# Kernel tuning notes

Measured on AMD Instinct MI355X. Metric: run time of the kernel, lower is better.

The kernel has to match this reference:

```python
import jax, jax.numpy as jnp
import numpy as np

# Dense grid configuration (B, D, H, W) and channels C = nPlanes
B, D, H, W = 4, 64, 64, 64
C = 32
N_ACTIVE = 400000
N_SITES = B * D * H * W  # 1048576


def setup_inputs() -> dict:
    key = jax.random.key(0)
    k1, k2 = jax.random.split(key)
    features = jax.random.normal(k1, (N_ACTIVE, C), dtype=jnp.float32)
    flat_idx = jax.random.randint(k2, (N_ACTIVE,), 0, N_SITES, dtype=jnp.int64)
    return {"features": features, "flat_idx": flat_idx}


def reference(features, flat_idx):
    # Scatter sparse voxel features into the dense grid.
    # features: [N_active, C]; flat_idx: [N_active] linear index into B*D*H*W sites.
    dense = jnp.zeros((N_SITES, C), dtype=features.dtype)
    dense = dense.at[flat_idx].add(features)  # active sites are unique -> add == set
    # [B*D*H*W, C] -> [B, C, D, H, W] to match SCN's NCDHW dense layout
    return dense.reshape(B, D, H, W, C).transpose(0, 4, 1, 2, 3)
```

## Files before the change

kernel.cpp:

```cpp
#include <hip/hip_runtime.h>


#define DHW_LOG2 18
#define DHW (1 << DHW_LOG2)
#define C_CH 32
#define N_SITES_TOTAL (4 * DHW)
#define SITES_PER_BLOCK 128
#define LDS_PAD 132

typedef float floatx4 __attribute__((ext_vector_type(4)));

__global__ __launch_bounds__(256) void init_head_kernel(int* __restrict__ head, int n)
{
    int t = blockIdx.x * blockDim.x + threadIdx.x;
    if (t < n) head[t] = -1;
}

__global__ __launch_bounds__(256) void build_chains_kernel(
    const int* __restrict__ flat_idx,
    int* __restrict__ head,
    int* __restrict__ next,
    int n_active)
{
    int i = blockIdx.x * blockDim.x + threadIdx.x;
    if (i >= n_active) return;
    int s = flat_idx[i];
    int prev = atomicExch(&head[s], i);
    next[i] = prev;
}

__global__ __launch_bounds__(256) void gather_kernel(
    const float* __restrict__ feats,
    const int* __restrict__ head,
    const int* __restrict__ next,
    float* __restrict__ out)
{
    __shared__ __align__(16) float lds[C_CH][LDS_PAD];

    const int t  = threadIdx.x;
    const int sl = t >> 1;
    const int h  = t & 1;
    const int S0 = blockIdx.x * SITES_PER_BLOCK;
    const int S  = S0 + sl;

    floatx4 a0 = (floatx4)0.f, a1 = (floatx4)0.f, a2 = (floatx4)0.f, a3 = (floatx4)0.f;

    int p = head[S];
    while (p != -1) {
        const floatx4* row = (const floatx4*)(feats + ((size_t)p * C_CH + h * 16));
        int pn = next[p];
        floatx4 f0 = row[0];
        floatx4 f1 = row[1];
        floatx4 f2 = row[2];
        floatx4 f3 = row[3];
        a0 += f0; a1 += f1; a2 += f2; a3 += f3;
        p = pn;
    }

    float acc[16] = {
        a0.x, a0.y, a0.z, a0.w,  a1.x, a1.y, a1.z, a1.w,
        a2.x, a2.y, a2.z, a2.w,  a3.x, a3.y, a3.z, a3.w };
    #pragma unroll
    for (int j = 0; j < 16; ++j)
        lds[h * 16 + j][sl] = acc[j];

    __syncthreads();

    const int b   = S0 >> DHW_LOG2;
    const int sp0 = S0 & (DHW - 1);
    #pragma unroll
    for (int it = 0; it < 4; ++it) {
        int q  = it * 256 + t;
        int c  = q >> 5;
        int i4 = q & 31;
        floatx4 v = *reinterpret_cast<const floatx4*>(&lds[c][i4 * 4]);
        floatx4* o = reinterpret_cast<floatx4*>(
            out + (((size_t)(b * C_CH + c)) << DHW_LOG2) + sp0 + i4 * 4);
        __builtin_nontemporal_store(v, o);
    }
}

__global__ __launch_bounds__(256) void zero_kernel(float4* __restrict__ out, int n4)
{
    int t = blockIdx.x * blockDim.x + threadIdx.x;
    if (t < n4) out[t] = make_float4(0.f, 0.f, 0.f, 0.f);
}

__global__ __launch_bounds__(256) void scatter_atomic_kernel(
    const float* __restrict__ feats,
    const int* __restrict__ flat_idx,
    float* __restrict__ out,
    int n_active)
{
    int t = blockIdx.x * blockDim.x + threadIdx.x;
    int i = t >> 5, c = t & 31;
    if (i >= n_active) return;
    int s = flat_idx[i];
    atomicAdd(&out[(((size_t)(s >> DHW_LOG2) * C_CH + c) << DHW_LOG2) + (s & (DHW - 1))],
              feats[(size_t)i * C_CH + c]);
}

extern "C" void kernel_launch(void* const* d_in, const int* in_sizes, int n_in,
                              void* d_out, int out_size, void* d_ws, size_t ws_size,
                              hipStream_t stream) {
    const float* feats = (const float*)d_in[0];
    const int*   idx   = (const int*)d_in[1];
    float*       out   = (float*)d_out;
    int n_active = in_sizes[1];

    size_t head_bytes = (size_t)N_SITES_TOTAL * sizeof(int);
    size_t next_bytes = (size_t)n_active * sizeof(int);

    if (ws_size >= head_bytes + next_bytes) {
        int* head = (int*)d_ws;
        int* next = (int*)((char*)d_ws + head_bytes);

        init_head_kernel<<<(N_SITES_TOTAL + 255) / 256, 256, 0, stream>>>(head, N_SITES_TOTAL);
        build_chains_kernel<<<(n_active + 255) / 256, 256, 0, stream>>>(idx, head, next, n_active);
        gather_kernel<<<N_SITES_TOTAL / SITES_PER_BLOCK, 256, 0, stream>>>(feats, head, next, out);
    } else {
        int n4 = out_size >> 2;
        zero_kernel<<<(n4 + 255) / 256, 256, 0, stream>>>((float4*)out, n4);
        int total = n_active * C_CH;
        scatter_atomic_kernel<<<(total + 255) / 256, 256, 0, stream>>>(feats, idx, out, n_active);
    }
}
```

Measured before the change: 201.8 us.

## Replace per-site linked lists with fixed-capacity buckets plus overflow chain

Replaces the atomicExch linked-list chains with per-site count arrays and 8-slot buckets, with a linked-list fallback for overflow. The gather kernel loads up to eight row indices with two vector loads and issues the feature loads independently. This removes the serial dependent next[] pointer chase. The cost is a larger workspace (32 MB of buckets), extra init work for the count array, and a bucket read for every site, including empty ones.

```diff
diff --git a/kernel.cpp b/kernel.cpp
--- a/kernel.cpp
+++ b/kernel.cpp
@@ -6,33 +6,48 @@
 #define C_CH 32
 #define N_SITES_TOTAL (4 * DHW)
 #define SITES_PER_BLOCK 128
+#define N_TILES (N_SITES_TOTAL / SITES_PER_BLOCK)
 #define LDS_PAD 132
+#define CAP 8
 
 typedef float floatx4 __attribute__((ext_vector_type(4)));
 
-__global__ __launch_bounds__(256) void init_head_kernel(int* __restrict__ head, int n)
+__global__ __launch_bounds__(256) void init_kernel(int* __restrict__ count,
+                                                   int* __restrict__ ovf_head)
 {
     int t = blockIdx.x * blockDim.x + threadIdx.x;
-    if (t < n) head[t] = -1;
+    if (t < N_SITES_TOTAL / 2) {
+        ((int2*)count)[t]    = make_int2(0, 0);
+        ((int2*)ovf_head)[t] = make_int2(-1, -1);
+    }
 }
 
-__global__ __launch_bounds__(256) void build_chains_kernel(
+__global__ __launch_bounds__(256) void fill_buckets_kernel(
     const int* __restrict__ flat_idx,
-    int* __restrict__ head,
-    int* __restrict__ next,
+    int* __restrict__ count,
+    int* __restrict__ bucket,
+    int* __restrict__ ovf_head,
+    int* __restrict__ ovf_next,
     int n_active)
 {
     int i = blockIdx.x * blockDim.x + threadIdx.x;
     if (i >= n_active) return;
     int s = flat_idx[i];
-    int prev = atomicExch(&head[s], i);
-    next[i] = prev;
+    int pos = atomicAdd(&count[s], 1);
+    if (pos < CAP) {
+        bucket[(size_t)s * CAP + pos] = i;
+    } else {
+        int prev = atomicExch(&ovf_head[s], i);
+        ovf_next[i] = prev;
+    }
 }
 
 __global__ __launch_bounds__(256) void gather_kernel(
     const float* __restrict__ feats,
-    const int* __restrict__ head,
-    const int* __restrict__ next,
+    const int* __restrict__ count,
+    const int* __restrict__ bucket,
+    const int* __restrict__ ovf_head,
+    const int* __restrict__ ovf_next,
     float* __restrict__ out)
 {
     __shared__ __align__(16) float lds[C_CH][LDS_PAD];
@@ -43,18 +58,38 @@
     const int S0 = blockIdx.x * SITES_PER_BLOCK;
     const int S  = S0 + sl;
 
+    int c = count[S];
+    const int4* bkt = (const int4*)(bucket + (size_t)S * CAP);
+    int4 b0 = bkt[0];
+    int4 b1 = bkt[1];
+
     floatx4 a0 = (floatx4)0.f, a1 = (floatx4)0.f, a2 = (floatx4)0.f, a3 = (floatx4)0.f;
 
-    int p = head[S];
-    while (p != -1) {
-        const floatx4* row = (const floatx4*)(feats + ((size_t)p * C_CH + h * 16));
-        int pn = next[p];
-        floatx4 f0 = row[0];
-        floatx4 f1 = row[1];
-        floatx4 f2 = row[2];
-        floatx4 f3 = row[3];
-        a0 += f0; a1 += f1; a2 += f2; a3 += f3;
-        p = pn;
+    const int rows[CAP] = { b0.x, b0.y, b0.z, b0.w, b1.x, b1.y, b1.z, b1.w };
+    #pragma unroll
+    for (int k = 0; k < CAP; ++k) {
+        if (k < c) {
+            const floatx4* row = (const floatx4*)(feats + ((size_t)rows[k] * C_CH + h * 16));
+            floatx4 f0 = row[0];
+            floatx4 f1 = row[1];
+            floatx4 f2 = row[2];
+            floatx4 f3 = row[3];
+            a0 += f0; a1 += f1; a2 += f2; a3 += f3;
+        }
+    }
+
+    if (c > CAP) {
+        int p = ovf_head[S];
+        while (p != -1) {
+            const floatx4* row = (const floatx4*)(feats + ((size_t)p * C_CH + h * 16));
+            int pn = ovf_next[p];
+            floatx4 f0 = row[0];
+            floatx4 f1 = row[1];
+            floatx4 f2 = row[2];
+            floatx4 f3 = row[3];
+            a0 += f0; a1 += f1; a2 += f2; a3 += f3;
+            p = pn;
+        }
     }
 
     float acc[16] = {
@@ -71,11 +106,11 @@
     #pragma unroll
     for (int it = 0; it < 4; ++it) {
         int q  = it * 256 + t;
-        int c  = q >> 5;
+        int cc = q >> 5;
         int i4 = q & 31;
-        floatx4 v = *reinterpret_cast<const floatx4*>(&lds[c][i4 * 4]);
+        floatx4 v = *reinterpret_cast<const floatx4*>(&lds[cc][i4 * 4]);
         floatx4* o = reinterpret_cast<floatx4*>(
-            out + (((size_t)(b * C_CH + c)) << DHW_LOG2) + sp0 + i4 * 4);
+            out + (((size_t)(b * C_CH + cc)) << DHW_LOG2) + sp0 + i4 * 4);
         __builtin_nontemporal_store(v, o);
     }
 }
@@ -108,16 +143,23 @@
     float*       out   = (float*)d_out;
     int n_active = in_sizes[1];
 
-    size_t head_bytes = (size_t)N_SITES_TOTAL * sizeof(int);
-    size_t next_bytes = (size_t)n_active * sizeof(int);
+    size_t count_bytes = (size_t)N_SITES_TOTAL * sizeof(int);
+    size_t head_bytes  = (size_t)N_SITES_TOTAL * sizeof(int);
+    size_t next_bytes  = ((size_t)n_active * sizeof(int) + 0xFFFFF) & ~(size_t)0xFFFFF;
+    size_t bucket_off  = count_bytes + head_bytes + next_bytes;
+    size_t bucket_bytes = (size_t)N_SITES_TOTAL * CAP * sizeof(int);
 
-    if (ws_size >= head_bytes + next_bytes) {
-        int* head = (int*)d_ws;
-        int* next = (int*)((char*)d_ws + head_bytes);
+    if (ws_size >= bucket_off + bucket_bytes) {
+        int* count    = (int*)d_ws;
+        int* ovf_head = (int*)((char*)d_ws + count_bytes);
+        int* ovf_next = (int*)((char*)d_ws + count_bytes + head_bytes);
+        int* bucket   = (int*)((char*)d_ws + bucket_off);
 
-        init_head_kernel<<<(N_SITES_TOTAL + 255) / 256, 256, 0, stream>>>(head, N_SITES_TOTAL);
-        build_chains_kernel<<<(n_active + 255) / 256, 256, 0, stream>>>(idx, head, next, n_active);
-        gather_kernel<<<N_SITES_TOTAL / SITES_PER_BLOCK, 256, 0, stream>>>(feats, head, next, out);
+        init_kernel<<<(N_SITES_TOTAL / 2 + 255) / 256, 256, 0, stream>>>(count, ovf_head);
+        fill_buckets_kernel<<<(n_active + 255) / 256, 256, 0, stream>>>(
+            idx, count, bucket, ovf_head, ovf_next, n_active);
+        gather_kernel<<<N_TILES, 256, 0, stream>>>(
+            feats, count, bucket, ovf_head, ovf_next, out);
     } else {
         int n4 = out_size >> 2;
         zero_kernel<<<(n4 + 255) / 256, 256, 0, stream>>>((float4*)out, n4);
```

Measured after the change: 228.2 us. +13.1%, slower.
